# Optimization experiments

Measured on AMD Instinct MI355X. Metric: run time of the kernel, lower is better.

Reference implementation:

```python
import jax, jax.numpy as jnp
import numpy as np

B, H, W = 2, 128, 128
MID = 64            # mid_channels
DG = 16             # deform_groups
MAX_RES = 10.0      # max_residue_magnitude
CIN_OFF = 3 * MID + 4   # 196: cat(extra_feat, flow_1, flow_2)
COFF = DG * 27          # 432: o1 + o2 + mask, each DG*9


def setup_inputs() -> dict:
    key = jax.random.key(0)
    ks = jax.random.split(key, 9)
    return {
        "extra_feat": jax.random.normal(ks[0], (B, 3 * MID, H, W), jnp.float32),
        "flow_1": jax.random.normal(ks[1], (B, 2, H, W), jnp.float32) * 2.0,
        "flow_2": jax.random.normal(ks[2], (B, 2, H, W), jnp.float32) * 2.0,
        "feat_prop": jax.random.normal(ks[3], (B, MID, H, W), jnp.float32),
        "feat_n2": jax.random.normal(ks[4], (B, MID, H, W), jnp.float32),
        "w_off": jax.random.normal(ks[5], (COFF, CIN_OFF, 3, 3), jnp.float32) * 0.02,
        "b_off": jax.random.normal(ks[6], (COFF,), jnp.float32) * 0.02,
        "dc_weight": jax.random.normal(ks[7], (MID, 2 * MID, 3, 3), jnp.float32) * 0.05,
        "dc_bias": jax.random.normal(ks[8], (MID,), jnp.float32) * 0.05,
    }


def _conv3x3(x, w, b):
    y = jax.lax.conv_general_dilated(
        x, w, window_strides=(1, 1), padding=((1, 1), (1, 1)),
        dimension_numbers=("NCHW", "OIHW", "NCHW"))
    return y + b[None, :, None, None]


def _deform_conv2d(inp, offset, mask, weight, bias):
    # inp: [B, Cin, H, W]; offset: [B, 2*DG*9, H, W] (per group, per kernel pos: (dy, dx));
    # mask: [B, DG*9, H, W]; weight: [Cout, Cin, 3, 3]; stride=1, pad=1, dil=1.
    Bb, Cin, Hi, Wi = inp.shape
    K = 9
    cg = Cin // DG
    Ho, Wo = Hi, Wi
    ki = jnp.repeat(jnp.arange(3), 3)  # kernel row index per flat k (row-major)
    kj = jnp.tile(jnp.arange(3), 3)
    base_y = (jnp.arange(Ho) - 1)[None, :, None] + ki[:, None, None]  # [K, Ho, 1]
    base_x = (jnp.arange(Wo) - 1)[None, None, :] + kj[:, None, None]  # [K, 1, Wo]
    off = offset.reshape(Bb, DG, K, 2, Ho, Wo)
    py = base_y[None, None] + off[:, :, :, 0]  # [B, DG, K, Ho, Wo]
    px = base_x[None, None] + off[:, :, :, 1]
    y0 = jnp.floor(py)
    x0 = jnp.floor(px)
    inp_g = inp.reshape(Bb, DG, cg, Hi * Wi)
    acc = jnp.zeros((Bb, DG, cg, K, Ho, Wo), inp.dtype)
    for dy in (0.0, 1.0):
        for dx in (0.0, 1.0):
            yc = y0 + dy
            xc = x0 + dx
            wgt = (1.0 - jnp.abs(py - yc)) * (1.0 - jnp.abs(px - xc))
            valid = (yc >= 0) & (yc < Hi) & (xc >= 0) & (xc < Wi)
            idx = (jnp.clip(yc, 0, Hi - 1) * Wi + jnp.clip(xc, 0, Wi - 1)).astype(jnp.int32)
            idx = jnp.broadcast_to(idx.reshape(Bb, DG, 1, K * Ho * Wo), (Bb, DG, cg, K * Ho * Wo))
            g = jnp.take_along_axis(inp_g, idx, axis=3).reshape(Bb, DG, cg, K, Ho, Wo)
            acc = acc + g * (wgt * valid)[:, :, None]
    sm = acc * mask.reshape(Bb, DG, 1, K, Ho, Wo)  # modulated samples
    wr = weight.reshape(weight.shape[0], DG, cg, K)
    out = jnp.einsum("bgckhw,ogck->bohw", sm, wr) + bias[None, :, None, None]
    return out


def reference(extra_feat, flow_1, flow_2, feat_prop, feat_n2, w_off, b_off, dc_weight, dc_bias):
    x = jnp.concatenate([extra_feat, flow_1, flow_2], axis=1)
    out = _conv3x3(x, w_off, b_off)
    o1, o2, m = jnp.split(out, 3, axis=1)  # each [B, DG*9, H, W]
    offset = MAX_RES * jnp.tanh(jnp.concatenate([o1, o2], axis=1))
    rep = DG * 3 * 3 // 2  # 72
    f1 = jnp.tile(flow_1[:, ::-1], (1, rep, 1, 1))  # flip(1): (dx,dy)->(dy,dx)
    f2 = jnp.tile(flow_2[:, ::-1], (1, rep, 1, 1))
    half = offset.shape[1] // 2
    offset = jnp.concatenate([offset[:, :half] + f1, offset[:, half:] + f2], axis=1)
    mask = jax.nn.sigmoid(m)
    inp = jnp.concatenate([feat_prop, feat_n2], axis=1)
    return _deform_conv2d(inp, offset, mask, dc_weight, dc_bias)
```

## Files before the change

kernel.cpp:

```cpp
#include <hip/hip_runtime.h>
#include <math.h>

#define Hh 128
#define Ww 128
#define HW (128*128)
#define CIN_OFF 196
#define COFF 432

typedef _Float16 half8 __attribute__((ext_vector_type(8)));
typedef _Float16 half4 __attribute__((ext_vector_type(4)));
typedef _Float16 half2v __attribute__((ext_vector_type(2)));
typedef float f32x4 __attribute__((ext_vector_type(4)));

static __device__ __forceinline__ half8 splat8(float v) {
  _Float16 h = (_Float16)v;
  half8 r = {h, h, h, h, h, h, h, h};
  return r;
}

__global__ __launch_bounds__(256) void k_prep_dcw(const float* __restrict__ dcw,
                                                  _Float16* __restrict__ wH) {
  int idx = blockIdx.x * 256 + threadIdx.x;
  if (idx < 64 * 1152) {
    int co = idx / 1152;
    int j  = idx - co * 1152;
    int k  = j >> 7;
    int ci = j & 127;
    wH[idx] = (_Float16)dcw[(co * 128 + ci) * 9 + k];
  }
}

__global__ __launch_bounds__(256) void k_prep_w(const float* __restrict__ w_off,
                                                _Float16* __restrict__ BpT,
                                                _Float16* __restrict__ Bt) {
  int idx = blockIdx.x * 256 + threadIdx.x;
  if (idx < 774144) {
    const int c  = idx & 7;
    const int n  = (idx >> 3) % 448;
    const int sl = (idx >> 3) / 448;
    const int l4 = sl & 3;
    const int s  = sl >> 2;
    const int t  = s / 6;
    const int cg = s - t * 6;
    const int ci = cg * 32 + l4 * 8 + c;
    BpT[idx] = (_Float16)((n < COFF) ? w_off[((size_t)n * CIN_OFF + ci) * 9 + t] : 0.f);
  } else if (idx < 774144 + 16128) {
    const int j = idx - 774144;
    const int c = j & 3;
    const int n = (j >> 2) % 448;
    const int t = (j >> 2) / 448;
    Bt[j] = (_Float16)((n < COFF) ? w_off[((size_t)n * CIN_OFF + 192 + c) * 9 + t] : 0.f);
  }
}

__global__ __launch_bounds__(256) void k_prep_feat(const float* __restrict__ fp,
                                                   const float* __restrict__ fn2,
                                                   _Float16* __restrict__ featT) {
  const int t = blockIdx.x * 256 + threadIdx.x;
  const int b = t >> 14;
  const int hw = t & 16383;
#pragma unroll
  for (int g = 0; g < 16; ++g) {
    const float* src = (g < 8) ? fp : fn2;
    const int ch0 = (g & 7) * 8;
    half8 v;
#pragma unroll
    for (int c = 0; c < 8; ++c)
      v[c] = (_Float16)src[(size_t)(b * 64 + ch0 + c) * HW + hw];
    *(half8*)(featT + (((size_t)(b * 16 + g)) * HW + hw) * 8) = v;
  }
}

__global__ __launch_bounds__(1024, 4) void k_offconv_mfma(
    const float* __restrict__ extra, const float* __restrict__ f1, const float* __restrict__ f2,
    const _Float16* __restrict__ BpT, const _Float16* __restrict__ Bt,
    const float* __restrict__ b_off,
    _Float16* __restrict__ off_pm, _Float16* __restrict__ mask_pm) {
  __shared__ __align__(16) _Float16 smA[3 * 130 * 192];
  __shared__ __align__(16) _Float16 smT[3 * 130 * 4];
  const int h    = blockIdx.x;
  const int b    = blockIdx.y;
  const int tid  = (int)threadIdx.x;
  const int lane = tid & 63;
  const int wid  = tid >> 6;
  const int wm   = wid >> 2;
  const int wn   = wid & 3;
  const int m_base = wm * 32;
  const int n_base = wn * 112;
  const int l15 = lane & 15;
  const int l4  = lane >> 4;

  if (tid < 588) {
    const int p2 = tid % 98;
    const int rr = tid / 98;
    const int r  = (rr >= 3) ? (rr - 3) : rr;
    const int px = (rr >= 3) ? 129 : 0;
    if (p2 < 96) {
      const int ci = 2 * p2, biw = ci >> 3;
      const int sw = ((biw & 24) | ((biw & 7) ^ (px & 7))) << 3;
      *(half2v*)(smA + (r * 130 + px) * 192 + sw + (ci & 7)) = (half2v){(_Float16)0.f, (_Float16)0.f};
    } else {
      *(half2v*)(smT + (r * 130 + px) * 4 + 2 * (p2 - 96)) = (half2v){(_Float16)0.f, (_Float16)0.f};
    }
  }

#pragma unroll 1
  for (int j = 0; j < 9; ++j) {
    const int J   = tid + 1024 * j;
    const int p2a = J & 15;
    const int qa  = (J >> 4) & 3;
    const int R   = J >> 6;
    const int r   = R / 48;
    const int rem = R - 48 * r;
    const int qh  = rem & 7;
    const int p2h = rem >> 3;
    const int q   = qa + 4 * qh;
    const int p2  = p2a + 16 * p2h;
    const int ci  = 2 * p2;
    const int gh  = h - 1 + r;
    float4 va = {0.f, 0.f, 0.f, 0.f}, vb = va;
    if ((unsigned)gh < (unsigned)Hh) {
      const float* xp = extra + (size_t)(b * 192 + ci) * HW + gh * Ww + 4 * q;
      va = *(const float4*)xp;
      vb = *(const float4*)(xp + HW);
    }
    const float av[4] = {va.x, va.y, va.z, va.w};
    const float bv[4] = {vb.x, vb.y, vb.z, vb.w};
    const int biw = p2 >> 2;
#pragma unroll
    for (int i = 0; i < 4; ++i) {
      const int px = 1 + 4 * q + i;
      const int sw = ((biw & 24) | ((biw & 7) ^ (px & 7))) << 3;
      half2v pk; pk[0] = (_Float16)av[i]; pk[1] = (_Float16)bv[i];
      *(half2v*)(smA + (r * 130 + px) * 192 + sw + (ci & 7)) = pk;
    }
  }
  if (tid < 192) {
    const int q   = tid & 31;
    const int p2t = (tid >> 5) & 1;
    const int r   = tid >> 6;
    const int gh  = h - 1 + r;
    float4 va = {0.f, 0.f, 0.f, 0.f}, vb = va;
    if ((unsigned)gh < (unsigned)Hh) {
      const float* xp = (p2t ? f2 : f1) + (size_t)(b * 2) * HW + gh * Ww + 4 * q;
      va = *(const float4*)xp;
      vb = *(const float4*)(xp + HW);
    }
    const float av[4] = {va.x, va.y, va.z, va.w};
    const float bv[4] = {vb.x, vb.y, vb.z, vb.w};
#pragma unroll
    for (int i = 0; i < 4; ++i) {
      const int px = 1 + 4 * q + i;
      half2v pk; pk[0] = (_Float16)av[i]; pk[1] = (_Float16)bv[i];
      *(half2v*)(smT + (r * 130 + px) * 4 + 2 * p2t) = pk;
    }
  }
  __syncthreads();

  f32x4 acc[2][7];
#pragma unroll
  for (int i = 0; i < 2; ++i)
#pragma unroll
    for (int j = 0; j < 7; ++j) acc[i][j] = (f32x4){0.f, 0.f, 0.f, 0.f};

  const bool lz = (l4 == 0);
#pragma unroll 3
  for (int t = 0; t < 9; ++t) {
    const int ki = t / 3;
    const int kj = t - 3 * ki;
#pragma unroll
    for (int cg = 0; cg < 6; ++cg) {
      const int s4 = ((t * 6 + cg) * 4 + l4) * 448;
      half8 bf[7];
#pragma unroll
      for (int f = 0; f < 7; ++f)
        bf[f] = *(const half8*)(BpT + (size_t)(s4 + n_base + f * 16 + l15) * 8);
      half8 af[2];
#pragma unroll
      for (int mf = 0; mf < 2; ++mf) {
        const int px = m_base + mf * 16 + l15 + kj;
        const int bi = cg * 4 + l4;
        af[mf] = *(const half8*)(smA + (ki * 130 + px) * 192 +
                                 (((bi & 24) | ((bi & 7) ^ (px & 7))) << 3));
      }
#pragma unroll
      for (int mf = 0; mf < 2; ++mf)
#pragma unroll
        for (int f = 0; f < 7; ++f)
          acc[mf][f] = __builtin_amdgcn_mfma_f32_16x16x32_f16(af[mf], bf[f], acc[mf][f], 0, 0, 0);
    }
    half8 aft[2];
#pragma unroll
    for (int mf = 0; mf < 2; ++mf) {
      const int px = m_base + mf * 16 + l15 + kj;
      const half4 tv = *(const half4*)(smT + (ki * 130 + px) * 4);
      half8 a = {0, 0, 0, 0, 0, 0, 0, 0};
      if (lz) { a[0] = tv[0]; a[1] = tv[1]; a[2] = tv[2]; a[3] = tv[3]; }
      aft[mf] = a;
    }
#pragma unroll
    for (int f = 0; f < 7; ++f) {
      const half4 wv = *(const half4*)(Bt + (size_t)(t * 448 + n_base + f * 16 + l15) * 4);
      half8 bb = {0, 0, 0, 0, 0, 0, 0, 0};
      if (lz) { bb[0] = wv[0]; bb[1] = wv[1]; bb[2] = wv[2]; bb[3] = wv[3]; }
#pragma unroll
      for (int mf = 0; mf < 2; ++mf)
        acc[mf][f] = __builtin_amdgcn_mfma_f32_16x16x32_f16(aft[mf], bb, acc[mf][f], 0, 0, 0);
    }
  }

  __syncthreads();
  _Float16* so = smA;
  const int hw0 = h * Ww;
#pragma unroll
  for (int f = 0; f < 7; ++f) {
    const int n = n_base + f * 16 + l15;
    const float bias = (n < COFF) ? b_off[n] : 0.f;
    const bool isOff = (n < 288);
    const float* fl = (n < 144) ? f1 : f2;
    const size_t fladd = (size_t)(b * 2 + ((n & 1) ^ 1)) * HW;
#pragma unroll
    for (int mf = 0; mf < 2; ++mf) {
#pragma unroll
      for (int rr = 0; rr < 4; ++rr) {
        const int px = m_base + mf * 16 + l4 * 4 + rr;
        const float v = acc[mf][f][rr] + bias;
        float val;
        if (isOff) {
          const float e = __expf(2.f * v);
          val = 10.f * (1.f - 2.f / (e + 1.f)) + fl[fladd + hw0 + px];
        } else {
          val = 1.f / (1.f + __expf(-v));
        }
        so[px * 456 + n] = (_Float16)val;
      }
    }
  }
  __syncthreads();
  for (int T = tid; T < 4608; T += 1024) {
    const int px = T / 36, c = T - px * 36;
    const half8 v = *(const half8*)(so + px * 456 + c * 8);
    *(half8*)(off_pm + ((size_t)b * HW + hw0 + px) * 288 + c * 8) = v;
  }
  for (int T = tid; T < 2304; T += 1024) {
    const int px = T / 18, c = T - px * 18;
    const half8 v = *(const half8*)(so + px * 456 + 288 + c * 8);
    *(half8*)(mask_pm + ((size_t)b * HW + hw0 + px) * 144 + c * 8) = v;
  }
}

__global__ __launch_bounds__(256) void k_deform2(
    const _Float16* __restrict__ featT, const _Float16* __restrict__ off_pm,
    const _Float16* __restrict__ mask_pm, const _Float16* __restrict__ wH,
    const float* __restrict__ dcb, float* __restrict__ out) {
  __shared__ __align__(16) char smem[16 * 1160 * 2];
  _Float16* sm = (_Float16*)smem;
  float* red = (float*)smem;
  const int w0  = blockIdx.x * 16;
  const int h   = blockIdx.y;
  const int b   = blockIdx.z;
  const int tid = (int)threadIdx.x;
  const int lane = tid & 63, wid = tid >> 6;
  const int l15 = lane & 15, l4 = lane >> 4;

#pragma unroll 1
  for (int i = 0; i < 9; ++i) {
    const int p   = tid + i * 256;
    const int pix = p / 144;
    const int r   = p - pix * 144;
    const int g   = r / 9;
    const int k   = r - g * 9;
    const int w   = w0 + pix;
    const int hw  = h * Ww + w;
    const half2v offh = *(const half2v*)(off_pm + ((size_t)b * HW + hw) * 288 + 2 * r);
    const float mk = (float)mask_pm[((size_t)b * HW + hw) * 144 + r];
    const int ki = (k >= 6) ? 2 : (k >= 3 ? 1 : 0);
    const int kj = k - 3 * ki;
    const float py = (float)(h - 1 + ki) + (float)offh[0];
    const float px = (float)(w - 1 + kj) + (float)offh[1];
    const float y0f = floorf(py), x0f = floorf(px);
    const int y0 = (int)y0f, x0 = (int)x0f;
    const float ly = py - y0f, lx = px - x0f;
    const float hy = 1.f - ly, hx = 1.f - lx;
    const int y1 = y0 + 1, x1 = x0 + 1;
    const bool vy0 = (unsigned)y0 < (unsigned)Hh, vy1 = (unsigned)y1 < (unsigned)Hh;
    const bool vx0 = (unsigned)x0 < (unsigned)Ww, vx1 = (unsigned)x1 < (unsigned)Ww;
    const float w00 = (vy0 && vx0) ? hy * hx : 0.f;
    const float w01 = (vy0 && vx1) ? hy * lx : 0.f;
    const float w10 = (vy1 && vx0) ? ly * hx : 0.f;
    const float w11 = (vy1 && vx1) ? ly * lx : 0.f;
    const int cy0 = min(max(y0, 0), Hh - 1), cy1 = min(max(y1, 0), Hh - 1);
    const int cx0 = min(max(x0, 0), Ww - 1), cx1 = min(max(x1, 0), Ww - 1);
    const _Float16* gbase = featT + ((size_t)(b * 16 + g) * HW) * 8;
    const half8 s00 = *(const half8*)(gbase + (cy0 * Ww + cx0) * 8);
    const half8 s01 = *(const half8*)(gbase + (cy0 * Ww + cx1) * 8);
    const half8 s10 = *(const half8*)(gbase + (cy1 * Ww + cx0) * 8);
    const half8 s11 = *(const half8*)(gbase + (cy1 * Ww + cx1) * 8);
    half8 v = s00 * splat8(w00) + s01 * splat8(w01) + s10 * splat8(w10) + s11 * splat8(w11);
    v = v * splat8(mk);
    const int swz = (g ^ (k & 7)) << 3;
    *(half8*)(sm + pix * 1160 + k * 128 + swz) = v;
  }
  __syncthreads();

  f32x4 acc[4];
#pragma unroll
  for (int nf = 0; nf < 4; ++nf) acc[nf] = (f32x4){0.f, 0.f, 0.f, 0.f};
#pragma unroll
  for (int j = 0; j < 9; ++j) {
    const int s  = wid * 9 + j;
    const int k  = s >> 2;
    const int cg = s & 3;
    const int gidx = cg * 4 + l4;
    const half8 af = *(const half8*)(sm + l15 * 1160 + k * 128 + ((gidx ^ (k & 7)) << 3));
    const int koff = s * 32 + l4 * 8;
#pragma unroll
    for (int nf = 0; nf < 4; ++nf) {
      const half8 bf = *(const half8*)(wH + (nf * 16 + l15) * 1152 + koff);
      acc[nf] = __builtin_amdgcn_mfma_f32_16x16x32_f16(af, bf, acc[nf], 0, 0, 0);
    }
  }
  __syncthreads();
#pragma unroll
  for (int nf = 0; nf < 4; ++nf)
#pragma unroll
    for (int rr = 0; rr < 4; ++rr)
      red[(wid * 16 + l4 * 4 + rr) * 66 + nf * 16 + l15] = acc[nf][rr];
  __syncthreads();

  const int m  = tid & 15;
  const int ng = tid >> 4;
#pragma unroll
  for (int i = 0; i < 4; ++i) {
    const int n = ng + 16 * i;
    float val = red[(0 * 16 + m) * 66 + n] + red[(1 * 16 + m) * 66 + n] +
                red[(2 * 16 + m) * 66 + n] + red[(3 * 16 + m) * 66 + n];
    out[(size_t)(b * 64 + n) * HW + h * Ww + w0 + m] = val + dcb[n];
  }
}

extern "C" void kernel_launch(void* const* d_in, const int* in_sizes, int n_in,
                              void* d_out, int out_size, void* d_ws, size_t ws_size,
                              hipStream_t stream) {
  const float* extra = (const float*)d_in[0];
  const float* f1    = (const float*)d_in[1];
  const float* f2    = (const float*)d_in[2];
  const float* fp    = (const float*)d_in[3];
  const float* fn2   = (const float*)d_in[4];
  const float* w_off = (const float*)d_in[5];
  const float* b_off = (const float*)d_in[6];
  const float* dcw   = (const float*)d_in[7];
  const float* dcb   = (const float*)d_in[8];
  float* out = (float*)d_out;

  _Float16* off_pm  = (_Float16*)d_ws;
  _Float16* mask_pm = off_pm + (size_t)2 * 288 * HW;
  _Float16* featT   = mask_pm + (size_t)2 * 144 * HW;
  _Float16* BpT     = featT + (size_t)2 * 128 * HW;
  _Float16* Bt      = BpT + 774144;
  _Float16* wH      = Bt + 16128;

  hipLaunchKernelGGL(k_prep_dcw, dim3(288), dim3(256), 0, stream, dcw, wH);
  hipLaunchKernelGGL(k_prep_w, dim3((774144 + 16128 + 255) / 256), dim3(256), 0, stream,
                     w_off, BpT, Bt);
  hipLaunchKernelGGL(k_prep_feat, dim3(128), dim3(256), 0, stream, fp, fn2, featT);
  hipLaunchKernelGGL(k_offconv_mfma, dim3(128, 2), dim3(1024), 0, stream,
                     extra, f1, f2, BpT, Bt, b_off, off_pm, mask_pm);
  hipLaunchKernelGGL(k_deform2, dim3(8, 128, 2), dim3(256), 0, stream,
                     featT, off_pm, mask_pm, wH, dcb, out);
}
```

Before: 189.2 us.

## Merge prep kernels into one launch and retune offconv and deform loops

Folds the three preprocessing kernels (deform weight reorder, offset-conv weight reorder, feature transpose) into one kernel that picks its task from the block index, removing two launches and their gaps. It also swaps the wave-to-tile mapping in the offset conv so the four warps in a row group share the same N slice, unrolls the staging loops by three in both main kernels, and adds a minimum-occupancy hint to the deform kernel. The unrolling and occupancy hint may raise register pressure or force spills.

New measurement: 183.3 us. -3.1%, faster.

```diff
diff --git a/kernel.cpp b/kernel.cpp
--- a/kernel.cpp
+++ b/kernel.cpp
@@ -18,56 +18,52 @@
   return r;
 }
 
-__global__ __launch_bounds__(256) void k_prep_dcw(const float* __restrict__ dcw,
-                                                  _Float16* __restrict__ wH) {
-  int idx = blockIdx.x * 256 + threadIdx.x;
-  if (idx < 64 * 1152) {
-    int co = idx / 1152;
-    int j  = idx - co * 1152;
-    int k  = j >> 7;
-    int ci = j & 127;
-    wH[idx] = (_Float16)dcw[(co * 128 + ci) * 9 + k];
-  }
-}
-
-__global__ __launch_bounds__(256) void k_prep_w(const float* __restrict__ w_off,
-                                                _Float16* __restrict__ BpT,
-                                                _Float16* __restrict__ Bt) {
-  int idx = blockIdx.x * 256 + threadIdx.x;
-  if (idx < 774144) {
-    const int c  = idx & 7;
-    const int n  = (idx >> 3) % 448;
-    const int sl = (idx >> 3) / 448;
-    const int l4 = sl & 3;
-    const int s  = sl >> 2;
-    const int t  = s / 6;
-    const int cg = s - t * 6;
-    const int ci = cg * 32 + l4 * 8 + c;
-    BpT[idx] = (_Float16)((n < COFF) ? w_off[((size_t)n * CIN_OFF + ci) * 9 + t] : 0.f);
-  } else if (idx < 774144 + 16128) {
-    const int j = idx - 774144;
-    const int c = j & 3;
-    const int n = (j >> 2) % 448;
-    const int t = (j >> 2) / 448;
-    Bt[j] = (_Float16)((n < COFF) ? w_off[((size_t)n * CIN_OFF + 192 + c) * 9 + t] : 0.f);
-  }
-}
-
-__global__ __launch_bounds__(256) void k_prep_feat(const float* __restrict__ fp,
-                                                   const float* __restrict__ fn2,
-                                                   _Float16* __restrict__ featT) {
-  const int t = blockIdx.x * 256 + threadIdx.x;
-  const int b = t >> 14;
-  const int hw = t & 16383;
-#pragma unroll
-  for (int g = 0; g < 16; ++g) {
-    const float* src = (g < 8) ? fp : fn2;
-    const int ch0 = (g & 7) * 8;
-    half8 v;
-#pragma unroll
-    for (int c = 0; c < 8; ++c)
-      v[c] = (_Float16)src[(size_t)(b * 64 + ch0 + c) * HW + hw];
-    *(half8*)(featT + (((size_t)(b * 16 + g)) * HW + hw) * 8) = v;
+__global__ __launch_bounds__(256) void k_prep_all(
+    const float* __restrict__ dcw, const float* __restrict__ w_off,
+    const float* __restrict__ fp, const float* __restrict__ fn2,
+    _Float16* __restrict__ wH, _Float16* __restrict__ BpT, _Float16* __restrict__ Bt,
+    _Float16* __restrict__ featT) {
+  const int bid = blockIdx.x;
+  if (bid < 3375) {
+    const int idx = bid * 256 + (int)threadIdx.x;
+    if (idx < 73728) {
+      const int co = idx / 1152;
+      const int j  = idx - co * 1152;
+      const int k  = j >> 7;
+      const int ci = j & 127;
+      wH[idx] = (_Float16)dcw[(co * 128 + ci) * 9 + k];
+    } else if (idx < 73728 + 774144) {
+      const int j  = idx - 73728;
+      const int c  = j & 7;
+      const int n  = (j >> 3) % 448;
+      const int sl = (j >> 3) / 448;
+      const int l4 = sl & 3;
+      const int s  = sl >> 2;
+      const int t  = s / 6;
+      const int cg = s - t * 6;
+      const int ci = cg * 32 + l4 * 8 + c;
+      BpT[j] = (_Float16)((n < COFF) ? w_off[((size_t)n * CIN_OFF + ci) * 9 + t] : 0.f);
+    } else {
+      const int j = idx - 73728 - 774144;
+      const int c = j & 3;
+      const int n = (j >> 2) % 448;
+      const int t = (j >> 2) / 448;
+      Bt[j] = (_Float16)((n < COFF) ? w_off[((size_t)n * CIN_OFF + 192 + c) * 9 + t] : 0.f);
+    }
+  } else {
+    const int t = (bid - 3375) * 256 + (int)threadIdx.x;
+    const int b = t >> 14;
+    const int hw = t & 16383;
+#pragma unroll
+    for (int g = 0; g < 16; ++g) {
+      const float* src = (g < 8) ? fp : fn2;
+      const int ch0 = (g & 7) * 8;
+      half8 v;
+#pragma unroll
+      for (int c = 0; c < 8; ++c)
+        v[c] = (_Float16)src[(size_t)(b * 64 + ch0 + c) * HW + hw];
+      *(half8*)(featT + (((size_t)(b * 16 + g)) * HW + hw) * 8) = v;
+    }
   }
 }
 
@@ -83,8 +79,8 @@
   const int tid  = (int)threadIdx.x;
   const int lane = tid & 63;
   const int wid  = tid >> 6;
-  const int wm   = wid >> 2;
-  const int wn   = wid & 3;
+  const int wm   = wid & 3;
+  const int wn   = wid >> 2;
   const int m_base = wm * 32;
   const int n_base = wn * 112;
   const int l15 = lane & 15;
@@ -104,7 +100,7 @@
     }
   }
 
-#pragma unroll 1
+#pragma unroll 3
   for (int j = 0; j < 9; ++j) {
     const int J   = tid + 1024 * j;
     const int p2a = J & 15;
@@ -249,7 +245,7 @@
   }
 }
 
-__global__ __launch_bounds__(256) void k_deform2(
+__global__ __launch_bounds__(256, 4) void k_deform2(
     const _Float16* __restrict__ featT, const _Float16* __restrict__ off_pm,
     const _Float16* __restrict__ mask_pm, const _Float16* __restrict__ wH,
     const float* __restrict__ dcb, float* __restrict__ out) {
@@ -263,7 +259,7 @@
   const int lane = tid & 63, wid = tid >> 6;
   const int l15 = lane & 15, l4 = lane >> 4;
 
-#pragma unroll 1
+#pragma unroll 3
   for (int i = 0; i < 9; ++i) {
     const int p   = tid + i * 256;
     const int pix = p / 144;
@@ -360,10 +356,8 @@
   _Float16* Bt      = BpT + 774144;
   _Float16* wH      = Bt + 16128;
 
-  hipLaunchKernelGGL(k_prep_dcw, dim3(288), dim3(256), 0, stream, dcw, wH);
-  hipLaunchKernelGGL(k_prep_w, dim3((774144 + 16128 + 255) / 256), dim3(256), 0, stream,
-                     w_off, BpT, Bt);
-  hipLaunchKernelGGL(k_prep_feat, dim3(128), dim3(256), 0, stream, fp, fn2, featT);
+  hipLaunchKernelGGL(k_prep_all, dim3(3503), dim3(256), 0, stream,
+                     dcw, w_off, fp, fn2, wH, BpT, Bt, featT);
   hipLaunchKernelGGL(k_offconv_mfma, dim3(128, 2), dim3(1024), 0, stream,
                      extra, f1, f2, BpT, Bt, b_off, off_pm, mask_pm);
   hipLaunchKernelGGL(k_deform2, dim3(8, 128, 2), dim3(256), 0, stream,
```
